# Optimization experiments

Measured on AMD Instinct MI355X. Metric: run time of the kernel, lower is better.

The kernel has to match this reference:

```python
import jax, jax.numpy as jnp
import numpy as np

N_NODES = 100000
N_EDGES = 400000
N_GRAPHS = 4096
IN_DIM = 128
HID = 64
HEADS = 8
NEG_SLOPE = 0.2


def setup_inputs() -> dict:
    key = jax.random.key(0)
    ks = jax.random.split(key, 12)
    x = jax.random.normal(ks[0], (N_NODES, IN_DIM), dtype=jnp.float32)
    edge_index = jax.random.randint(ks[1], (2, N_EDGES), 0, N_NODES, dtype=jnp.int64)
    batch = jnp.sort(jax.random.randint(ks[2], (N_NODES,), 0, N_GRAPHS, dtype=jnp.int64))
    s = 1.0 / np.sqrt(IN_DIM)
    W1 = jax.random.normal(ks[3], (IN_DIM, HEADS * HID), dtype=jnp.float32) * s
    att_src1 = jax.random.normal(ks[4], (HEADS, HID), dtype=jnp.float32) * 0.1
    att_dst1 = jax.random.normal(ks[5], (HEADS, HID), dtype=jnp.float32) * 0.1
    b1 = jnp.zeros((HEADS * HID,), dtype=jnp.float32)
    s2 = 1.0 / np.sqrt(HEADS * HID)
    W2 = jax.random.normal(ks[6], (HEADS * HID, HID), dtype=jnp.float32) * s2
    att_src2 = jax.random.normal(ks[7], (1, HID), dtype=jnp.float32) * 0.1
    att_dst2 = jax.random.normal(ks[8], (1, HID), dtype=jnp.float32) * 0.1
    b2 = jnp.zeros((HID,), dtype=jnp.float32)
    Wf = jax.random.normal(ks[9], (HID, 1), dtype=jnp.float32) * (1.0 / np.sqrt(HID))
    bf = jnp.zeros((1,), dtype=jnp.float32)
    return {"x": x, "edge_index": edge_index, "batch": batch,
            "W1": W1, "att_src1": att_src1, "att_dst1": att_dst1, "b1": b1,
            "W2": W2, "att_src2": att_src2, "att_dst2": att_dst2, "b2": b2,
            "Wf": Wf, "bf": bf}


def _gat_layer(x, src, dst, W, att_src, att_dst, bias, heads, out_ch, concat):
    # PyG GATConv math (add_self_loops handled by caller via src/dst)
    n = x.shape[0]
    h = (x @ W).reshape(n, heads, out_ch)          # [N, H, C]
    a_s = (h * att_src[None]).sum(-1)               # [N, H]
    a_d = (h * att_dst[None]).sum(-1)               # [N, H]
    alpha = a_s[src] + a_d[dst]                     # [E, H]
    alpha = jax.nn.leaky_relu(alpha, NEG_SLOPE)
    amax = jax.ops.segment_max(alpha, dst, num_segments=n)
    alpha = jnp.exp(alpha - amax[dst])
    denom = jax.ops.segment_sum(alpha, dst, num_segments=n)
    alpha = alpha / (denom[dst] + 1e-16)
    msg = h[src] * alpha[:, :, None]                # [E, H, C]
    out = jax.ops.segment_sum(msg, dst, num_segments=n)  # [N, H, C]
    out = out.reshape(n, heads * out_ch) if concat else out.mean(axis=1)
    return out + bias


def reference(x, edge_index, batch, W1, att_src1, att_dst1, b1,
              W2, att_src2, att_dst2, b2, Wf, bf):
    n = x.shape[0]
    loop = jnp.arange(n, dtype=edge_index.dtype)
    src = jnp.concatenate([edge_index[0], loop])
    dst = jnp.concatenate([edge_index[1], loop])
    h = _gat_layer(x, src, dst, W1, att_src1, att_dst1, b1, HEADS, HID, True)
    h = jax.nn.relu(h)
    h = _gat_layer(h, src, dst, W2, att_src2, att_dst2, b2, 1, HID, False)
    h = jax.nn.relu(h)
    sums = jax.ops.segment_sum(h, batch, num_segments=N_GRAPHS)        # [G, HID]
    cnts = jax.ops.segment_sum(jnp.ones((n,), h.dtype), batch, num_segments=N_GRAPHS)
    pooled = sums / jnp.clip(cnts, 1.0)[:, None]
    return pooled @ Wf + bf
```

## Files before the change

kernel.cpp:

```cpp
#include <hip/hip_runtime.h>

typedef short bfrag8 __attribute__((ext_vector_type(8)));
typedef float f32x4 __attribute__((ext_vector_type(4)));
typedef unsigned int uint4v __attribute__((ext_vector_type(4)));

#define SCAN_BLK 2048

__device__ __forceinline__ unsigned short f2bf(float f) {
    unsigned u = __float_as_uint(f);
    u += 0x7fffu + ((u >> 16) & 1u);
    return (unsigned short)(u >> 16);
}
__device__ __forceinline__ float bf2f(unsigned short s) {
    return __uint_as_float((unsigned)s << 16);
}
__device__ __forceinline__ bfrag8 pack8(float4 a, float4 b) {
    bfrag8 r;
    r[0] = (short)f2bf(a.x); r[1] = (short)f2bf(a.y);
    r[2] = (short)f2bf(a.z); r[3] = (short)f2bf(a.w);
    r[4] = (short)f2bf(b.x); r[5] = (short)f2bf(b.y);
    r[6] = (short)f2bf(b.z); r[7] = (short)f2bf(b.w);
    return r;
}

__global__ __launch_bounds__(256) void prologue(int* __restrict__ cnt,
                                                const float* __restrict__ W1,
                                                const float* __restrict__ W2,
                                                unsigned short* __restrict__ wf1,
                                                unsigned short* __restrict__ wf2,
                                                const float* __restrict__ bf,
                                                float* __restrict__ out,
                                                const int* __restrict__ batch,
                                                int* __restrict__ gstart,
                                                int* __restrict__ rs,
                                                int N, int G, int E) {
    const int b = blockIdx.x, t = threadIdx.x;
    if (b < 512) {
        int i = b * 256 + t;
        if (i < N) cnt[i] = 0;
    } else if (b < 768) {
        int i = (b - 512) * 256 + t;
        int e = i & 7, l = (i >> 3) & 63, c = (i >> 9) & 3, s = (i >> 11) & 3, h = i >> 13;
        int k = s * 32 + (l >> 4) * 8 + e;
        int col = h * 64 + c * 16 + (l & 15);
        wf1[i] = f2bf(W1[k * 512 + col]);
    } else if (b < 896) {
        int i = (b - 768) * 256 + t;
        int e = i & 7, l = (i >> 3) & 63, c = (i >> 9) & 3, s = i >> 11;
        int k = s * 32 + (l >> 4) * 8 + e;
        int col = c * 16 + (l & 15);
        wf2[i] = f2bf(W2[k * 64 + col]);
    } else if (b < 912) {
        int i = (b - 896) * 256 + t;
        if (i < G) out[i] = bf[0];
    } else {
        int i = (b - 912) * 256 + t;
        if (i == 0) rs[N] = E + N;
        if (i > N) return;
        if (i == N) {
            int p = batch[N - 1];
            for (int g = p + 1; g <= G; ++g) gstart[g] = N;
        } else {
            int bb = batch[i];
            int p = (i == 0) ? -1 : batch[i - 1];
            for (int g = p + 1; g <= bb; ++g) gstart[g] = i;
        }
    }
}

__global__ __launch_bounds__(256) void gemm_l1_hist(const float* __restrict__ x,
                                                    const unsigned short* __restrict__ Bfrag,
                                                    unsigned short* __restrict__ Cbf,
                                                    int M,
                                                    const float* __restrict__ avs,
                                                    const float* __restrict__ avd,
                                                    float* __restrict__ as_,
                                                    float* __restrict__ ad_,
                                                    int gemmBlocks,
                                                    const int* __restrict__ ei,
                                                    int* __restrict__ cnt, int E) {
    const int b = blockIdx.x;
    if (b >= gemmBlocks) {
        int t = (b - gemmBlocks) * 256 + threadIdx.x;
        if (t < E + M) {
            int dst = (t < E) ? ei[E + t] : t - E;
            atomicAdd(cnt + dst, 1);
        }
        return;
    }
    const int lane = threadIdx.x & 63;
    const int wave = threadIdx.x >> 6;
    const int l15 = lane & 15, l16 = lane >> 4;
    const long rowBase = (long)b * 128 + wave * 32;

    long r0 = rowBase + l15;        if (r0 > M - 1) r0 = M - 1;
    long r1 = rowBase + 16 + l15;   if (r1 > M - 1) r1 = M - 1;

    bfrag8 a0f[4], a1f[4];
#pragma unroll
    for (int s = 0; s < 4; ++s) {
        const float* p0 = x + r0 * 128 + s * 32 + l16 * 8;
        const float* p1 = x + r1 * 128 + s * 32 + l16 * 8;
        float4 u0 = *(const float4*)p0, u1 = *(const float4*)(p0 + 4);
        float4 v0 = *(const float4*)p1, v1 = *(const float4*)(p1 + 4);
        a0f[s] = pack8(u0, u1);
        a1f[s] = pack8(v0, v1);
    }

#pragma unroll 1
    for (int h = 0; h < 8; ++h) {
        bfrag8 bf[4][4];
        const bfrag8* bp = (const bfrag8*)(Bfrag + (size_t)h * 8192);
#pragma unroll
        for (int s = 0; s < 4; ++s)
#pragma unroll
            for (int c = 0; c < 4; ++c)
                bf[s][c] = bp[(s * 4 + c) * 64 + lane];

        f32x4 acc[2][4];
#pragma unroll
        for (int r = 0; r < 2; ++r)
#pragma unroll
            for (int c = 0; c < 4; ++c)
#pragma unroll
                for (int e = 0; e < 4; ++e) acc[r][c][e] = 0.f;

#pragma unroll
        for (int s = 0; s < 4; ++s) {
#pragma unroll
            for (int c = 0; c < 4; ++c) {
                acc[0][c] = __builtin_amdgcn_mfma_f32_16x16x32_bf16(a0f[s], bf[s][c], acc[0][c], 0, 0, 0);
                acc[1][c] = __builtin_amdgcn_mfma_f32_16x16x32_bf16(a1f[s], bf[s][c], acc[1][c], 0, 0, 0);
            }
        }

        float avsv[4], avdv[4];
#pragma unroll
        for (int c = 0; c < 4; ++c) {
            avsv[c] = avs[h * 64 + c * 16 + l15];
            avdv[c] = avd[h * 64 + c * 16 + l15];
        }

#pragma unroll
        for (int r = 0; r < 2; ++r) {
#pragma unroll
            for (int reg = 0; reg < 4; ++reg) {
                long row = rowBase + r * 16 + l16 * 4 + reg;
                bool ok = row < M;
                float ps = 0.f, pd = 0.f;
#pragma unroll
                for (int c = 0; c < 4; ++c) {
                    float v = acc[r][c][reg];
                    if (ok) Cbf[row * 512 + h * 64 + c * 16 + l15] = f2bf(v);
                    ps += v * avsv[c];
                    pd += v * avdv[c];
                }
#pragma unroll
                for (int off = 1; off < 16; off <<= 1) {
                    ps += __shfl_xor(ps, off);
                    pd += __shfl_xor(pd, off);
                }
                if (l15 == 0 && ok) {
                    as_[row * 8 + h] = ps;
                    ad_[row * 8 + h] = pd;
                }
            }
        }
    }
}

__global__ __launch_bounds__(256) void scan1(const int* __restrict__ cnt,
                                             int* __restrict__ rs,
                                             int* __restrict__ bsum, int N) {
    __shared__ int lds[256];
    int base = blockIdx.x * SCAN_BLK;
    int vals[8];
    int tsum = 0;
    int idx0 = base + threadIdx.x * 8;
#pragma unroll
    for (int j = 0; j < 8; ++j) {
        int i = idx0 + j;
        int v = (i < N) ? cnt[i] : 0;
        vals[j] = tsum;
        tsum += v;
    }
    lds[threadIdx.x] = tsum;
    __syncthreads();
    for (int off = 1; off < 256; off <<= 1) {
        int v = lds[threadIdx.x];
        int u = (threadIdx.x >= (unsigned)off) ? lds[threadIdx.x - off] : 0;
        __syncthreads();
        lds[threadIdx.x] = v + u;
        __syncthreads();
    }
    int texcl = (threadIdx.x == 0) ? 0 : lds[threadIdx.x - 1];
#pragma unroll
    for (int j = 0; j < 8; ++j) {
        int i = idx0 + j;
        if (i < N) rs[i] = texcl + vals[j];
    }
    if (threadIdx.x == 255) bsum[blockIdx.x] = lds[255];
}

__global__ __launch_bounds__(256) void scan_fix(int* __restrict__ rs,
                                                const int* __restrict__ bsum, int N) {
    __shared__ int sprefix;
    int b = blockIdx.x;
    int i = b * 256 + threadIdx.x;
    int chunk = (b * 256) / SCAN_BLK;
    if (threadIdx.x == 0) {
        int p = 0;
        for (int k = 0; k < chunk; ++k) p += bsum[k];
        sprefix = p;
    }
    __syncthreads();
    if (i < N) rs[i] += sprefix;
}

__global__ __launch_bounds__(256) void scatter_cd(const int* __restrict__ ei,
                                                  const int* __restrict__ rs,
                                                  int* __restrict__ cnt,
                                                  int* __restrict__ csrc, int E, int N) {
    int t = (int)(blockIdx.x * 256u + threadIdx.x);
    if (t >= E + N) return;
    int src, dst;
    if (t < E) { src = ei[t]; dst = ei[E + t]; } else { src = dst = t - E; }
    int pos = rs[dst] + atomicSub(cnt + dst, 1) - 1;
    csrc[pos] = src;
}

__global__ __launch_bounds__(256) void gather8(const int* __restrict__ csrc,
                                               const int* __restrict__ rs,
                                               const float* __restrict__ as_,
                                               const float* __restrict__ ad_,
                                               const unsigned short* __restrict__ h,
                                               const float* __restrict__ bias,
                                               unsigned short* __restrict__ outp,
                                               int N) {
    int node = (int)((blockIdx.x * 256u + threadIdx.x) >> 6);
    int lane = threadIdx.x & 63;
    if (node >= N) return;
    int myh = lane >> 3;
    int s0 = rs[node], s1 = rs[node + 1];
    float adn = ad_[(size_t)node * 8 + myh];
    float den = 0.f;
    float2 acc[4] = {};
    const unsigned* hu = (const unsigned*)h;
    int k = s0;
    for (; k + 4 <= s1; k += 4) {
        int i0 = csrc[k], i1 = csrc[k + 1], i2 = csrc[k + 2], i3 = csrc[k + 3];
        float a0 = as_[(size_t)i0 * 8 + myh] + adn;
        float a1 = as_[(size_t)i1 * 8 + myh] + adn;
        float a2 = as_[(size_t)i2 * 8 + myh] + adn;
        float a3 = as_[(size_t)i3 * 8 + myh] + adn;
        a0 = a0 > 0.f ? a0 : 0.2f * a0;  a1 = a1 > 0.f ? a1 : 0.2f * a1;
        a2 = a2 > 0.f ? a2 : 0.2f * a2;  a3 = a3 > 0.f ? a3 : 0.2f * a3;
        float w0 = __expf(fminf(a0, 60.f)), w1 = __expf(fminf(a1, 60.f));
        float w2 = __expf(fminf(a2, 60.f)), w3 = __expf(fminf(a3, 60.f));
        uint4v v0 = *(const uint4v*)(hu + (size_t)i0 * 256 + lane * 4);
        uint4v v1 = *(const uint4v*)(hu + (size_t)i1 * 256 + lane * 4);
        uint4v v2 = *(const uint4v*)(hu + (size_t)i2 * 256 + lane * 4);
        uint4v v3 = *(const uint4v*)(hu + (size_t)i3 * 256 + lane * 4);
        den += (w0 + w1) + (w2 + w3);
#pragma unroll
        for (int j = 0; j < 4; ++j) {
            acc[j].x += w0 * __uint_as_float(v0[j] << 16);
            acc[j].y += w0 * __uint_as_float(v0[j] & 0xffff0000u);
            acc[j].x += w1 * __uint_as_float(v1[j] << 16);
            acc[j].y += w1 * __uint_as_float(v1[j] & 0xffff0000u);
            acc[j].x += w2 * __uint_as_float(v2[j] << 16);
            acc[j].y += w2 * __uint_as_float(v2[j] & 0xffff0000u);
            acc[j].x += w3 * __uint_as_float(v3[j] << 16);
            acc[j].y += w3 * __uint_as_float(v3[j] & 0xffff0000u);
        }
    }
    for (; k < s1; ++k) {
        int i0 = csrc[k];
        float a = as_[(size_t)i0 * 8 + myh] + adn;
        a = a > 0.f ? a : 0.2f * a;
        float w = __expf(fminf(a, 60.f));
        uint4v v0 = *(const uint4v*)(hu + (size_t)i0 * 256 + lane * 4);
        den += w;
#pragma unroll
        for (int j = 0; j < 4; ++j) {
            acc[j].x += w * __uint_as_float(v0[j] << 16);
            acc[j].y += w * __uint_as_float(v0[j] & 0xffff0000u);
        }
    }
    float rden = 1.f / (den + 1e-16f);
    uint4v o;
#pragma unroll
    for (int j = 0; j < 4; ++j) {
        float vlo = acc[j].x * rden + bias[lane * 8 + 2 * j];
        float vhi = acc[j].y * rden + bias[lane * 8 + 2 * j + 1];
        vlo = vlo > 0.f ? vlo : 0.f;
        vhi = vhi > 0.f ? vhi : 0.f;
        o[j] = (unsigned)f2bf(vlo) | ((unsigned)f2bf(vhi) << 16);
    }
    *(uint4v*)(outp + (size_t)node * 512 + lane * 8) = o;
}

__global__ __launch_bounds__(256) void gemm_l2_k512(const unsigned short* __restrict__ A,
                                                    const unsigned short* __restrict__ Bfrag,
                                                    unsigned short* __restrict__ Cbf,
                                                    int M,
                                                    const float* __restrict__ avs,
                                                    const float* __restrict__ avd,
                                                    float* __restrict__ as_,
                                                    float* __restrict__ ad_) {
    const int lane = threadIdx.x & 63;
    const int wave = threadIdx.x >> 6;
    const int l15 = lane & 15, l16 = lane >> 4;
    const long rowBase = (long)blockIdx.x * 128 + wave * 32;
    const bfrag8* bp = (const bfrag8*)Bfrag;

    f32x4 acc[2][4];
#pragma unroll
    for (int r = 0; r < 2; ++r)
#pragma unroll
        for (int c = 0; c < 4; ++c)
#pragma unroll
            for (int e = 0; e < 4; ++e) acc[r][c][e] = 0.f;

    long r0 = rowBase + l15;        if (r0 > M - 1) r0 = M - 1;
    long r1 = rowBase + 16 + l15;   if (r1 > M - 1) r1 = M - 1;
    const unsigned short* a0p = A + r0 * 512 + l16 * 8;
    const unsigned short* a1p = A + r1 * 512 + l16 * 8;

    for (int s = 0; s < 16; ++s) {
        bfrag8 a0 = *(const bfrag8*)(a0p + s * 32);
        bfrag8 a1 = *(const bfrag8*)(a1p + s * 32);
        bfrag8 bf0 = bp[(s * 4 + 0) * 64 + lane];
        bfrag8 bf1 = bp[(s * 4 + 1) * 64 + lane];
        bfrag8 bf2 = bp[(s * 4 + 2) * 64 + lane];
        bfrag8 bf3 = bp[(s * 4 + 3) * 64 + lane];
        acc[0][0] = __builtin_amdgcn_mfma_f32_16x16x32_bf16(a0, bf0, acc[0][0], 0, 0, 0);
        acc[1][0] = __builtin_amdgcn_mfma_f32_16x16x32_bf16(a1, bf0, acc[1][0], 0, 0, 0);
        acc[0][1] = __builtin_amdgcn_mfma_f32_16x16x32_bf16(a0, bf1, acc[0][1], 0, 0, 0);
        acc[1][1] = __builtin_amdgcn_mfma_f32_16x16x32_bf16(a1, bf1, acc[1][1], 0, 0, 0);
        acc[0][2] = __builtin_amdgcn_mfma_f32_16x16x32_bf16(a0, bf2, acc[0][2], 0, 0, 0);
        acc[1][2] = __builtin_amdgcn_mfma_f32_16x16x32_bf16(a1, bf2, acc[1][2], 0, 0, 0);
        acc[0][3] = __builtin_amdgcn_mfma_f32_16x16x32_bf16(a0, bf3, acc[0][3], 0, 0, 0);
        acc[1][3] = __builtin_amdgcn_mfma_f32_16x16x32_bf16(a1, bf3, acc[1][3], 0, 0, 0);
    }

    float avsv[4], avdv[4];
#pragma unroll
    for (int c = 0; c < 4; ++c) {
        avsv[c] = avs[c * 16 + l15];
        avdv[c] = avd[c * 16 + l15];
    }

#pragma unroll
    for (int r = 0; r < 2; ++r) {
#pragma unroll
        for (int reg = 0; reg < 4; ++reg) {
            long row = rowBase + r * 16 + l16 * 4 + reg;
            bool ok = row < M;
            float ps = 0.f, pd = 0.f;
#pragma unroll
            for (int c = 0; c < 4; ++c) {
                float v = acc[r][c][reg];
                if (ok) Cbf[row * 64 + c * 16 + l15] = f2bf(v);
                ps += v * avsv[c];
                pd += v * avdv[c];
            }
#pragma unroll
            for (int off = 1; off < 16; off <<= 1) {
                ps += __shfl_xor(ps, off);
                pd += __shfl_xor(pd, off);
            }
            if (l15 == 0 && ok) { as_[row] = ps; ad_[row] = pd; }
        }
    }
}

__global__ __launch_bounds__(256) void gather1_pool(const int* __restrict__ csrc,
                                                    const int* __restrict__ rs,
                                                    const float* __restrict__ as_,
                                                    const float* __restrict__ ad_,
                                                    const unsigned short* __restrict__ h,
                                                    const float* __restrict__ bias,
                                                    const int* __restrict__ batch,
                                                    const int* __restrict__ gstart,
                                                    const float* __restrict__ Wf,
                                                    float* __restrict__ out, int N) {
    int node = (int)((blockIdx.x * 256u + threadIdx.x) >> 6);
    int lane = threadIdx.x & 63;
    if (node >= N) return;
    int s0 = rs[node], s1 = rs[node + 1];
    float adn = ad_[node];
    float den = 0.f, acc = 0.f;
    int k = s0;
    for (; k + 4 <= s1; k += 4) {
        int i0 = csrc[k], i1 = csrc[k + 1], i2 = csrc[k + 2], i3 = csrc[k + 3];
        float a0 = as_[i0] + adn, a1 = as_[i1] + adn, a2 = as_[i2] + adn, a3 = as_[i3] + adn;
        a0 = a0 > 0.f ? a0 : 0.2f * a0;  a1 = a1 > 0.f ? a1 : 0.2f * a1;
        a2 = a2 > 0.f ? a2 : 0.2f * a2;  a3 = a3 > 0.f ? a3 : 0.2f * a3;
        float w0 = __expf(fminf(a0, 60.f)), w1 = __expf(fminf(a1, 60.f));
        float w2 = __expf(fminf(a2, 60.f)), w3 = __expf(fminf(a3, 60.f));
        float h0 = bf2f(h[(size_t)i0 * 64 + lane]);
        float h1 = bf2f(h[(size_t)i1 * 64 + lane]);
        float h2 = bf2f(h[(size_t)i2 * 64 + lane]);
        float h3 = bf2f(h[(size_t)i3 * 64 + lane]);
        den += (w0 + w1) + (w2 + w3);
        acc += w0 * h0;  acc += w1 * h1;  acc += w2 * h2;  acc += w3 * h3;
    }
    for (; k < s1; ++k) {
        int i0 = csrc[k];
        float a = as_[i0] + adn;
        a = a > 0.f ? a : 0.2f * a;
        float w = __expf(fminf(a, 60.f));
        den += w;
        acc += w * bf2f(h[(size_t)i0 * 64 + lane]);
    }
    float v = acc / (den + 1e-16f) + bias[lane];
    v = v > 0.f ? v : 0.f;
    float s = v * Wf[lane];
#pragma unroll
    for (int off = 32; off; off >>= 1) s += __shfl_xor(s, off);
    if (lane == 0) {
        int b = batch[node];
        float cnt = (float)(gstart[b + 1] - gstart[b]);
        atomicAdd(out + b, s / cnt);
    }
}

extern "C" void kernel_launch(void* const* d_in, const int* in_sizes, int n_in,
                              void* d_out, int out_size, void* d_ws, size_t ws_size,
                              hipStream_t stream) {
    const float* x        = (const float*)d_in[0];
    const int*   ei       = (const int*)d_in[1];
    const int*   batch    = (const int*)d_in[2];
    const float* W1       = (const float*)d_in[3];
    const float* att_src1 = (const float*)d_in[4];
    const float* att_dst1 = (const float*)d_in[5];
    const float* b1       = (const float*)d_in[6];
    const float* W2       = (const float*)d_in[7];
    const float* att_src2 = (const float*)d_in[8];
    const float* att_dst2 = (const float*)d_in[9];
    const float* b2       = (const float*)d_in[10];
    const float* Wf       = (const float*)d_in[11];
    const float* bf       = (const float*)d_in[12];
    float* out = (float*)d_out;

    const int N = in_sizes[2];
    const int E = in_sizes[1] / 2;
    const int G = out_size;

    const int nb = (N + SCAN_BLK - 1) / SCAN_BLK;
    const int nodeWaveGrid = (int)(((size_t)N * 64 + 255) / 256);
    const int edgeGrid = (E + N + 255) / 256;
    const int gemmGrid = (N + 127) / 128;

    char* base = (char*)d_ws;
    size_t off = 0;
    auto alloc = [&](size_t bytes) { char* p = base + off; off += (bytes + 255) & ~255llu; return p; };
    unsigned short* wf1   = (unsigned short*)alloc(131072);
    unsigned short* wf2   = (unsigned short*)alloc(65536);
    float* as1            = (float*)alloc((size_t)N * 8 * 4);
    float* ad1            = (float*)alloc((size_t)N * 8 * 4);
    float* as2            = (float*)alloc((size_t)N * 4);
    float* ad2            = (float*)alloc((size_t)N * 4);
    int*   cnt_i          = (int*)alloc((size_t)N * 4);
    int*   rs             = (int*)alloc((size_t)(N + 1) * 4);
    int*   csrc           = (int*)alloc((size_t)(E + N) * 4);
    int*   bsum           = (int*)alloc(1024);
    int*   gstart         = (int*)alloc((size_t)(G + 1) * 4);
    unsigned short* h2bf  = (unsigned short*)alloc((size_t)N * 64 * 2);
    unsigned short* h1_bf = (unsigned short*)alloc((size_t)N * 512 * 2);
    unsigned short* ob1_bf= (unsigned short*)alloc((size_t)N * 512 * 2);
    (void)ws_size;

    {
        int gsBlocks = (N + 256) / 256 + 1;
        prologue<<<912 + gsBlocks, 256, 0, stream>>>(cnt_i, W1, W2, wf1, wf2,
                                                     bf, out, batch, gstart, rs, N, G, E);
    }

    gemm_l1_hist<<<gemmGrid + edgeGrid, 256, 0, stream>>>(
        x, wf1, h1_bf, N, att_src1, att_dst1, as1, ad1,
        gemmGrid, ei, cnt_i, E);

    scan1<<<nb, 256, 0, stream>>>(cnt_i, rs, bsum, N);
    scan_fix<<<(N + 255) / 256, 256, 0, stream>>>(rs, bsum, N);
    scatter_cd<<<edgeGrid, 256, 0, stream>>>(ei, rs, cnt_i, csrc, E, N);

    gather8<<<nodeWaveGrid, 256, 0, stream>>>(csrc, rs, as1, ad1, h1_bf, b1, ob1_bf, N);

    gemm_l2_k512<<<gemmGrid, 256, 0, stream>>>(ob1_bf, wf2, h2bf, N,
                                               att_src2, att_dst2, as2, ad2);

    gather1_pool<<<nodeWaveGrid, 256, 0, stream>>>(csrc, rs, as2, ad2, h2bf, b2,
                                                   batch, gstart, Wf, out, N);
}
```

Before: 297.0 us.

## Split layer-1 gather into per-half-head passes and replace atomic pooling with segmented readout

The layer-1 aggregation now runs as two launches, each covering four heads. Each pass gathers 256 bf16 columns per neighbour instead of 512, which shrinks the per-pass working set in the h1 gather and may improve cache hit rates, at the cost of reading the CSR and attention scores twice. The layer-2 gather now writes fp32 node features to a new buffer, and a separate pool_readout kernel averages each graph's contiguous node range. This replaces the per-node atomicAdd into the output, trading the atomics for an extra kernel and a 25 MB write and read.

```diff
diff --git a/kernel.cpp b/kernel.cpp
--- a/kernel.cpp
+++ b/kernel.cpp
@@ -2,6 +2,7 @@
 
 typedef short bfrag8 __attribute__((ext_vector_type(8)));
 typedef float f32x4 __attribute__((ext_vector_type(4)));
+typedef unsigned int uint2v __attribute__((ext_vector_type(2)));
 typedef unsigned int uint4v __attribute__((ext_vector_type(4)));
 
 #define SCAN_BLK 2048
@@ -28,8 +29,6 @@
                                                 const float* __restrict__ W2,
                                                 unsigned short* __restrict__ wf1,
                                                 unsigned short* __restrict__ wf2,
-                                                const float* __restrict__ bf,
-                                                float* __restrict__ out,
                                                 const int* __restrict__ batch,
                                                 int* __restrict__ gstart,
                                                 int* __restrict__ rs,
@@ -50,11 +49,8 @@
         int k = s * 32 + (l >> 4) * 8 + e;
         int col = c * 16 + (l & 15);
         wf2[i] = f2bf(W2[k * 64 + col]);
-    } else if (b < 912) {
+    } else {
         int i = (b - 896) * 256 + t;
-        if (i < G) out[i] = bf[0];
-    } else {
-        int i = (b - 912) * 256 + t;
         if (i == 0) rs[N] = E + N;
         if (i > N) return;
         if (i == N) {
@@ -229,23 +225,25 @@
     csrc[pos] = src;
 }
 
-__global__ __launch_bounds__(256) void gather8(const int* __restrict__ csrc,
-                                               const int* __restrict__ rs,
-                                               const float* __restrict__ as_,
-                                               const float* __restrict__ ad_,
-                                               const unsigned short* __restrict__ h,
-                                               const float* __restrict__ bias,
-                                               unsigned short* __restrict__ outp,
-                                               int N) {
+template<int HALF>
+__global__ __launch_bounds__(256) void gather8_half(const int* __restrict__ csrc,
+                                                    const int* __restrict__ rs,
+                                                    const float* __restrict__ as_,
+                                                    const float* __restrict__ ad_,
+                                                    const unsigned short* __restrict__ h,
+                                                    const float* __restrict__ bias,
+                                                    unsigned short* __restrict__ outp,
+                                                    int N) {
     int node = (int)((blockIdx.x * 256u + threadIdx.x) >> 6);
     int lane = threadIdx.x & 63;
     if (node >= N) return;
-    int myh = lane >> 3;
+    const int myh = HALF * 4 + (lane >> 4);
     int s0 = rs[node], s1 = rs[node + 1];
     float adn = ad_[(size_t)node * 8 + myh];
     float den = 0.f;
-    float2 acc[4] = {};
+    float2 acc[2] = {};
     const unsigned* hu = (const unsigned*)h;
+    const unsigned rowoff = HALF * 128 + lane * 2;
     int k = s0;
     for (; k + 4 <= s1; k += 4) {
         int i0 = csrc[k], i1 = csrc[k + 1], i2 = csrc[k + 2], i3 = csrc[k + 3];
@@ -257,13 +255,13 @@
         a2 = a2 > 0.f ? a2 : 0.2f * a2;  a3 = a3 > 0.f ? a3 : 0.2f * a3;
         float w0 = __expf(fminf(a0, 60.f)), w1 = __expf(fminf(a1, 60.f));
         float w2 = __expf(fminf(a2, 60.f)), w3 = __expf(fminf(a3, 60.f));
-        uint4v v0 = *(const uint4v*)(hu + (size_t)i0 * 256 + lane * 4);
-        uint4v v1 = *(const uint4v*)(hu + (size_t)i1 * 256 + lane * 4);
-        uint4v v2 = *(const uint4v*)(hu + (size_t)i2 * 256 + lane * 4);
-        uint4v v3 = *(const uint4v*)(hu + (size_t)i3 * 256 + lane * 4);
+        uint2v v0 = *(const uint2v*)(hu + (size_t)i0 * 256 + rowoff);
+        uint2v v1 = *(const uint2v*)(hu + (size_t)i1 * 256 + rowoff);
+        uint2v v2 = *(const uint2v*)(hu + (size_t)i2 * 256 + rowoff);
+        uint2v v3 = *(const uint2v*)(hu + (size_t)i3 * 256 + rowoff);
         den += (w0 + w1) + (w2 + w3);
 #pragma unroll
-        for (int j = 0; j < 4; ++j) {
+        for (int j = 0; j < 2; ++j) {
             acc[j].x += w0 * __uint_as_float(v0[j] << 16);
             acc[j].y += w0 * __uint_as_float(v0[j] & 0xffff0000u);
             acc[j].x += w1 * __uint_as_float(v1[j] << 16);
@@ -279,25 +277,25 @@
         float a = as_[(size_t)i0 * 8 + myh] + adn;
         a = a > 0.f ? a : 0.2f * a;
         float w = __expf(fminf(a, 60.f));
-        uint4v v0 = *(const uint4v*)(hu + (size_t)i0 * 256 + lane * 4);
+        uint2v v0 = *(const uint2v*)(hu + (size_t)i0 * 256 + rowoff);
         den += w;
 #pragma unroll
-        for (int j = 0; j < 4; ++j) {
+        for (int j = 0; j < 2; ++j) {
             acc[j].x += w * __uint_as_float(v0[j] << 16);
             acc[j].y += w * __uint_as_float(v0[j] & 0xffff0000u);
         }
     }
     float rden = 1.f / (den + 1e-16f);
-    uint4v o;
-#pragma unroll
-    for (int j = 0; j < 4; ++j) {
-        float vlo = acc[j].x * rden + bias[lane * 8 + 2 * j];
-        float vhi = acc[j].y * rden + bias[lane * 8 + 2 * j + 1];
+    uint2v o;
+#pragma unroll
+    for (int j = 0; j < 2; ++j) {
+        float vlo = acc[j].x * rden + bias[HALF * 256 + lane * 4 + 2 * j];
+        float vhi = acc[j].y * rden + bias[HALF * 256 + lane * 4 + 2 * j + 1];
         vlo = vlo > 0.f ? vlo : 0.f;
         vhi = vhi > 0.f ? vhi : 0.f;
         o[j] = (unsigned)f2bf(vlo) | ((unsigned)f2bf(vhi) << 16);
     }
-    *(uint4v*)(outp + (size_t)node * 512 + lane * 8) = o;
+    *(uint2v*)(outp + (size_t)node * 512 + HALF * 256 + lane * 4) = o;
 }
 
 __global__ __launch_bounds__(256) void gemm_l2_k512(const unsigned short* __restrict__ A,
@@ -375,16 +373,13 @@
     }
 }
 
-__global__ __launch_bounds__(256) void gather1_pool(const int* __restrict__ csrc,
-                                                    const int* __restrict__ rs,
-                                                    const float* __restrict__ as_,
-                                                    const float* __restrict__ ad_,
-                                                    const unsigned short* __restrict__ h,
-                                                    const float* __restrict__ bias,
-                                                    const int* __restrict__ batch,
-                                                    const int* __restrict__ gstart,
-                                                    const float* __restrict__ Wf,
-                                                    float* __restrict__ out, int N) {
+__global__ __launch_bounds__(256) void gather1(const int* __restrict__ csrc,
+                                               const int* __restrict__ rs,
+                                               const float* __restrict__ as_,
+                                               const float* __restrict__ ad_,
+                                               const unsigned short* __restrict__ h,
+                                               const float* __restrict__ bias,
+                                               float* __restrict__ outp, int N) {
     int node = (int)((blockIdx.x * 256u + threadIdx.x) >> 6);
     int lane = threadIdx.x & 63;
     if (node >= N) return;
@@ -415,15 +410,31 @@
         acc += w * bf2f(h[(size_t)i0 * 64 + lane]);
     }
     float v = acc / (den + 1e-16f) + bias[lane];
-    v = v > 0.f ? v : 0.f;
-    float s = v * Wf[lane];
-#pragma unroll
-    for (int off = 32; off; off >>= 1) s += __shfl_xor(s, off);
-    if (lane == 0) {
-        int b = batch[node];
-        float cnt = (float)(gstart[b + 1] - gstart[b]);
-        atomicAdd(out + b, s / cnt);
-    }
+    outp[(size_t)node * 64 + lane] = v > 0.f ? v : 0.f;
+}
+
+__global__ __launch_bounds__(256) void pool_readout(const float* __restrict__ h2,
+                                                    const int* __restrict__ gstart,
+                                                    const float* __restrict__ Wf,
+                                                    const float* __restrict__ bf,
+                                                    float* __restrict__ out, int G) {
+    int g = (int)((blockIdx.x * 256u + threadIdx.x) >> 6);
+    int lane = threadIdx.x & 63;
+    if (g >= G) return;
+    int s0 = gstart[g], s1 = gstart[g + 1];
+    float acc = 0.f;
+    int i = s0;
+    for (; i + 2 <= s1; i += 2) {
+        acc += h2[(size_t)i * 64 + lane];
+        acc += h2[(size_t)(i + 1) * 64 + lane];
+    }
+    if (i < s1) acc += h2[(size_t)i * 64 + lane];
+    float c = (float)(s1 - s0);
+    c = c < 1.f ? 1.f : c;
+    float v = acc / c * Wf[lane];
+#pragma unroll
+    for (int off = 32; off; off >>= 1) v += __shfl_xor(v, off);
+    if (lane == 0) out[g] = v + bf[0];
 }
 
 extern "C" void kernel_launch(void* const* d_in, const int* in_sizes, int n_in,
@@ -467,6 +478,7 @@
     int*   csrc           = (int*)alloc((size_t)(E + N) * 4);
     int*   bsum           = (int*)alloc(1024);
     int*   gstart         = (int*)alloc((size_t)(G + 1) * 4);
+    float* ob2            = (float*)alloc((size_t)N * 64 * 4);
     unsigned short* h2bf  = (unsigned short*)alloc((size_t)N * 64 * 2);
     unsigned short* h1_bf = (unsigned short*)alloc((size_t)N * 512 * 2);
     unsigned short* ob1_bf= (unsigned short*)alloc((size_t)N * 512 * 2);
@@ -474,8 +486,8 @@
 
     {
         int gsBlocks = (N + 256) / 256 + 1;
-        prologue<<<912 + gsBlocks, 256, 0, stream>>>(cnt_i, W1, W2, wf1, wf2,
-                                                     bf, out, batch, gstart, rs, N, G, E);
+        prologue<<<896 + gsBlocks, 256, 0, stream>>>(cnt_i, W1, W2, wf1, wf2,
+                                                     batch, gstart, rs, N, G, E);
     }
 
     gemm_l1_hist<<<gemmGrid + edgeGrid, 256, 0, stream>>>(
@@ -486,11 +498,13 @@
     scan_fix<<<(N + 255) / 256, 256, 0, stream>>>(rs, bsum, N);
     scatter_cd<<<edgeGrid, 256, 0, stream>>>(ei, rs, cnt_i, csrc, E, N);
 
-    gather8<<<nodeWaveGrid, 256, 0, stream>>>(csrc, rs, as1, ad1, h1_bf, b1, ob1_bf, N);
+    gather8_half<0><<<nodeWaveGrid, 256, 0, stream>>>(csrc, rs, as1, ad1, h1_bf, b1, ob1_bf, N);
+    gather8_half<1><<<nodeWaveGrid, 256, 0, stream>>>(csrc, rs, as1, ad1, h1_bf, b1, ob1_bf, N);
 
     gemm_l2_k512<<<gemmGrid, 256, 0, stream>>>(ob1_bf, wf2, h2bf, N,
                                                att_src2, att_dst2, as2, ad2);
 
-    gather1_pool<<<nodeWaveGrid, 256, 0, stream>>>(csrc, rs, as2, ad2, h2bf, b2,
-                                                   batch, gstart, Wf, out, N);
-}
+    gather1<<<nodeWaveGrid, 256, 0, stream>>>(csrc, rs, as2, ad2, h2bf, b2, ob2, N);
+
+    pool_readout<<<(G * 64 + 255) / 256, 256, 0, stream>>>(ob2, gstart, Wf, bf, out, G);
+}
```

Measured after the change: 288.7 us. -2.8%, faster.
